# Performance work log

Hardware: AMD Instinct MI355X
Metric: run time of the kernel (lower is better)

Reference implementation:

```python
import jax, jax.numpy as jnp
import numpy as np

SEQ, D, H = 4096, 1024, 16
HD = D // H
SCALE = HD ** -0.5


def setup_inputs() -> dict:
    key = jax.random.key(0)
    ks = jax.random.split(key, 8)
    s = 0.02
    return {
        "hidden_states": jax.random.normal(ks[0], (SEQ, D), dtype=jnp.float32),
        "wq": jax.random.normal(ks[1], (D, D), dtype=jnp.float32) * s,
        "bq": jax.random.normal(ks[2], (D,), dtype=jnp.float32) * s,
        "wk": jax.random.normal(ks[3], (D, D), dtype=jnp.float32) * s,
        "wv": jax.random.normal(ks[4], (D, D), dtype=jnp.float32) * s,
        "bv": jax.random.normal(ks[5], (D,), dtype=jnp.float32) * s,
        "wo": jax.random.normal(ks[6], (D, D), dtype=jnp.float32) * s,
        "bo": jax.random.normal(ks[7], (D,), dtype=jnp.float32) * s,
    }


def reference(hidden_states, wq, bq, wk, wv, bv, wo, bo):
    S = hidden_states.shape[0]
    # torch Linear: y = x @ W^T + b  (k_proj has no bias)
    q = (hidden_states @ wq.T + bq).reshape(S, H, HD).transpose(1, 0, 2)  # [H,S,hd]
    k = (hidden_states @ wk.T).reshape(S, H, HD).transpose(1, 0, 2)       # [H,S,hd]
    v = (hidden_states @ wv.T + bv).reshape(S, H, HD).transpose(1, 0, 2)  # [H,S,hd]
    scores = jnp.einsum('hqd,hkd->hqk', q, k) * SCALE                     # [H,S,S]
    # softmax computed in fp32 then cast back to query dtype
    attn = jax.nn.softmax(scores.astype(jnp.float32), axis=-1).astype(q.dtype)
    out = jnp.einsum('hqk,hkd->hqd', attn, v)                             # [H,S,hd]
    out = out.transpose(1, 0, 2).reshape(S, D)
    return out @ wo.T + bo
```

## Files before the change

### kernel.cpp

```cpp
#include <hip/hip_runtime.h>

#define SEQ 4096
#define DIM 1024
#define NH 16
#define HD 64
#define QKVSTR 3072

typedef __attribute__((ext_vector_type(8))) short bf16x8;
typedef __attribute__((ext_vector_type(4))) float f32x4;
typedef __attribute__((ext_vector_type(16))) float f32x16;
typedef __attribute__((ext_vector_type(4))) unsigned int uint4v;

__device__ __forceinline__ unsigned short f2bf(float f) {
  unsigned int b = __float_as_uint(f);
  b = b + 0x7fffu + ((b >> 16) & 1u);
  return (unsigned short)(b >> 16);
}

__device__ __forceinline__ unsigned int cvt_pk_bf16(float lo, float hi) {
  unsigned int r;
  asm("v_cvt_pk_bf16_f32 %0, %1, %2" : "=v"(r) : "v"(lo), "v"(hi));
  return r;
}

__device__ __forceinline__ float fast_exp2(float x) {
#if __has_builtin(__builtin_amdgcn_exp2f)
  return __builtin_amdgcn_exp2f(x);
#else
  float r; asm("v_exp_f32 %0, %1" : "=v"(r) : "v"(x)); return r;
#endif
}

typedef __attribute__((address_space(3))) unsigned int lds_uint;
typedef __attribute__((address_space(1))) const unsigned int global_uint;

__device__ __forceinline__ void gload_lds16(const void* g, void* l) {
  __builtin_amdgcn_global_load_lds((global_uint*)g, (lds_uint*)l, 16, 0, 0);
}

__global__ __launch_bounds__(256) void cast_all_kernel(
    const float* __restrict__ X, const float* __restrict__ wq, const float* __restrict__ wk,
    const float* __restrict__ wv, const float* __restrict__ wo,
    unsigned short* __restrict__ Xb, unsigned short* __restrict__ Wqkv,
    unsigned short* __restrict__ Wob, float qscale) {
  int i = blockIdx.x * 256 + threadIdx.x;
  const float* src;
  unsigned short* dst;
  float sc = 1.f;
  if (i < 524288) { src = X + (size_t)i * 8; dst = Xb + (size_t)i * 8; }
  else if (i < 655360) { int j = i - 524288; src = wq + (size_t)j * 8; dst = Wqkv + (size_t)j * 8; sc = qscale; }
  else if (i < 786432) { int j = i - 655360; src = wk + (size_t)j * 8; dst = Wqkv + 1048576 + (size_t)j * 8; }
  else if (i < 917504) { int j = i - 786432; src = wv + (size_t)j * 8; dst = Wqkv + 2097152 + (size_t)j * 8; }
  else { int j = i - 917504; src = wo + (size_t)j * 8; dst = Wob + (size_t)j * 8; }
  const float4* p = (const float4*)src;
  float4 x0 = p[0], x1 = p[1];
  union { unsigned short u[8]; uint4v v; } o;
  o.u[0] = f2bf(x0.x * sc); o.u[1] = f2bf(x0.y * sc);
  o.u[2] = f2bf(x0.z * sc); o.u[3] = f2bf(x0.w * sc);
  o.u[4] = f2bf(x1.x * sc); o.u[5] = f2bf(x1.y * sc);
  o.u[6] = f2bf(x1.z * sc); o.u[7] = f2bf(x1.w * sc);
  *(uint4v*)dst = o.v;
}

template<int BIASMODE, int OUT_F32, int BN>
__global__ __launch_bounds__(256) void gemm_bt_kernel(
    const unsigned short* __restrict__ A, const unsigned short* __restrict__ B,
    const float* __restrict__ b0, const float* __restrict__ b1, float qscale,
    void* __restrict__ Cout, unsigned short* __restrict__ Vt, int M, int N, int K) {
  constexpr int NF = BN / 32;
  __shared__ unsigned short As[3][128 * 32];
  __shared__ unsigned short Bs[3][BN * 32];
  int tid = threadIdx.x;
  int wave = tid >> 6, lane = tid & 63;
  int g = lane >> 4, lc = lane & 15;
  int wm = wave >> 1, wn = wave & 1;

  int gx = gridDim.x;
  int wgid = blockIdx.y * gx + blockIdx.x;
  int cpx = (gx * gridDim.y) >> 3;
  int sw = (wgid & 7) * cpx + (wgid >> 3);
  int m0 = (sw / gx) * 128, n0 = (sw % gx) * BN;

  int ch0 = wave * 64 + lane;
  int r0 = ch0 >> 2, cb0 = ch0 & 3;
  int ch1 = 256 + ch0;
  int r1 = ch1 >> 2, cb1 = ch1 & 3;
  const unsigned short* Ar0 = A + (size_t)(m0 + r0) * K + cb0 * 8;
  const unsigned short* Ar1 = A + (size_t)(m0 + r1) * K + cb1 * 8;
  const unsigned short* Br0 = B + (size_t)(n0 + r0) * K + cb0 * 8;
  const unsigned short* Br1 = B + (size_t)(n0 + r1) * K + cb1 * 8;

  unsigned short* sAlo[3] = { &As[0][(wave * 64) * 8], &As[1][(wave * 64) * 8], &As[2][(wave * 64) * 8] };
  unsigned short* sAhi[3] = { &As[0][(256 + wave * 64) * 8], &As[1][(256 + wave * 64) * 8], &As[2][(256 + wave * 64) * 8] };
  unsigned short* sBlo[3] = { &Bs[0][(wave * 64) * 8], &Bs[1][(wave * 64) * 8], &Bs[2][(wave * 64) * 8] };
  unsigned short* sBhi[3] = { &Bs[0][(256 + wave * 64) * 8], &Bs[1][(256 + wave * 64) * 8], &Bs[2][(256 + wave * 64) * 8] };

  f32x4 acc[4][NF] = {};

  auto stage = [&](int kn, int b) {
    gload_lds16(Ar0 + kn, sAlo[b]);
    gload_lds16(Ar1 + kn, sAhi[b]);
    gload_lds16(Br0 + kn, sBlo[b]);
    if (BN == 128) gload_lds16(Br1 + kn, sBhi[b]);
  };

  auto compute = [&](int b) {
    bf16x8 af[4], bfr[NF];
    for (int mf = 0; mf < 4; ++mf)
      af[mf] = *(const bf16x8*)&As[b][(wm * 64 + mf * 16 + lc) * 32 + g * 8];
    for (int nf = 0; nf < NF; ++nf)
      bfr[nf] = *(const bf16x8*)&Bs[b][(wn * (BN / 2) + nf * 16 + lc) * 32 + g * 8];
    for (int mf = 0; mf < 4; ++mf)
      for (int nf = 0; nf < NF; ++nf)
        acc[mf][nf] = __builtin_amdgcn_mfma_f32_16x16x32_bf16(af[mf], bfr[nf], acc[mf][nf], 0, 0, 0);
  };

  const int NT = K / 32;
  auto step = [&](int i, int CUR, int STG) {
    int kn = (i + 2 < NT) ? (i + 2) * 32 : 0;
    stage(kn, STG);
    if (BN == 128) {
      asm volatile("s_waitcnt vmcnt(8)" ::: "memory");
    } else {
      asm volatile("s_waitcnt vmcnt(6)" ::: "memory");
    }
    __builtin_amdgcn_sched_barrier(0);
    __builtin_amdgcn_s_barrier();
    __builtin_amdgcn_sched_barrier(0);
    compute(CUR);
    asm volatile("" ::: "memory");
    __builtin_amdgcn_sched_barrier(0);
    __builtin_amdgcn_s_barrier();
  };

  stage(0, 0);
  stage(32, 1);

  for (int ii = 0; ii < 30; ii += 3) {
    step(ii + 0, 0, 2);
    step(ii + 1, 1, 0);
    step(ii + 2, 2, 1);
  }
  step(30, 0, 2);
  step(31, 1, 0);

  for (int nf = 0; nf < NF; ++nf) {
    int col = n0 + wn * (BN / 2) + nf * 16 + lc;
    float bias = 0.f;
    if (BIASMODE == 1) {
      int sect = col >> 10, cc = col & 1023;
      bias = (sect == 0) ? b0[cc] * qscale : ((sect == 2) ? b1[cc] : 0.f);
    } else if (BIASMODE == 2) {
      bias = b0[col];
    }
    for (int mf = 0; mf < 4; ++mf) {
      int row = m0 + wm * 64 + mf * 16 + g * 4;
      for (int r = 0; r < 4; ++r) {
        float v = acc[mf][nf][r] + bias;
        if (OUT_F32) {
          ((float*)Cout)[(size_t)(row + r) * N + col] = v;
        } else if (BIASMODE == 1 && col >= 2048) {
          Vt[(size_t)(col - 2048) * SEQ + row + r] = f2bf(v);
        } else {
          ((unsigned short*)Cout)[(size_t)(row + r) * N + col] = f2bf(v);
        }
      }
    }
  }
}

__global__ __launch_bounds__(512, 1) void attn_kernel(
    const unsigned short* __restrict__ QKV, const unsigned short* __restrict__ Vt,
    unsigned short* __restrict__ Aout) {
  __shared__ unsigned short Qs[128 * 64];
  __shared__ unsigned short Ks[2][2][64 * 64];
  __shared__ unsigned short Vs[2][2][64 * 64];
  int tid = threadIdx.x;
  int w = tid >> 6, lane = tid & 63;
  int hi = lane >> 5, l31 = lane & 31;
  int qw = w & 3, grp = w >> 2;

  int bid = blockIdx.x;
  int swz = (bid & 7) * 64 + (bid >> 3);
  int h = swz >> 5;
  int q0 = (swz & 31) * 128;

  const unsigned short* Qg = QKV + h * HD;
  const unsigned short* Kg = QKV + DIM + h * HD;
  const unsigned short* Vg = Vt + (size_t)(h * HD) * SEQ;
  int kvbase = grp * (SEQ / 2);

  int ch0 = qw * 64 + lane;
  int r0s = ch0 >> 3, d0s = (ch0 & 7) ^ (r0s & 7);
  int ch1 = 256 + ch0;
  int r1s = ch1 >> 3, d1s = (ch1 & 7) ^ (r1s & 7);
  size_t koff0 = (size_t)r0s * QKVSTR + d0s * 8;
  size_t koff1 = (size_t)r1s * QKVSTR + d1s * 8;
  size_t voff0 = (size_t)r0s * SEQ + d0s * 8;
  size_t voff1 = (size_t)r1s * SEQ + d1s * 8;
  unsigned short* sKlo[2] = { &Ks[grp][0][(qw * 64) * 8],       &Ks[grp][1][(qw * 64) * 8] };
  unsigned short* sKhi[2] = { &Ks[grp][0][(256 + qw * 64) * 8], &Ks[grp][1][(256 + qw * 64) * 8] };
  unsigned short* sVlo[2] = { &Vs[grp][0][(qw * 64) * 8],       &Vs[grp][1][(qw * 64) * 8] };
  unsigned short* sVhi[2] = { &Vs[grp][0][(256 + qw * 64) * 8], &Vs[grp][1][(256 + qw * 64) * 8] };

  for (int c = 0; c < 2; ++c) {
    int chunk = c * 512 + w * 64 + lane;
    int row = chunk >> 3, pos = chunk & 7;
    int db = pos ^ (row & 7);
    gload_lds16(Qg + (size_t)(q0 + row) * QKVSTR + db * 8, Qs + (c * 512 + w * 64) * 8);
  }
  {
    const unsigned short* Kt = Kg + (size_t)kvbase * QKVSTR;
    const unsigned short* Vtt = Vg + kvbase;
    gload_lds16(Kt + koff0, sKlo[0]);
    gload_lds16(Kt + koff1, sKhi[0]);
    gload_lds16(Vtt + voff0, sVlo[0]);
    gload_lds16(Vtt + voff1, sVhi[0]);
  }
  asm volatile("s_waitcnt vmcnt(4)" ::: "memory");
  __builtin_amdgcn_sched_barrier(0);
  __builtin_amdgcn_s_barrier();

  bf16x8 qf[4];
  {
    int qrow = qw * 32 + l31;
    for (int dc = 0; dc < 4; ++dc) {
      int pos = 2 * dc + hi;
      qf[dc] = *(const bf16x8*)&Qs[qrow * 64 + (pos ^ (qrow & 7)) * 8];
    }
  }

  int offb[4];
#pragma unroll
  for (int dc = 0; dc < 4; ++dc)
    offb[dc] = l31 * 128 + (((2 * dc + hi) ^ (l31 & 7)) * 16);
  const char* KbA = (const char*)&Ks[grp][0][0];
  const char* KbB = (const char*)&Ks[grp][1][0];
  const char* VbA = (const char*)&Vs[grp][0][0];
  const char* VbB = (const char*)&Vs[grp][1][0];

  f32x16 o0 = {}, o1 = {};
  float la0 = 0.f, la1 = 0.f, la2 = 0.f, la3 = 0.f;

  auto body = [&](int t, int CUR) {
    int NB = CUR ^ 1;
    int kvn = kvbase + (((t + 1) & 31) << 6);
    const unsigned short* Kt = Kg + (size_t)kvn * QKVSTR;
    const unsigned short* Vtt = Vg + kvn;
    gload_lds16(Kt + koff0, sKlo[NB]);
    gload_lds16(Kt + koff1, sKhi[NB]);
    gload_lds16(Vtt + voff0, sVlo[NB]);
    gload_lds16(Vtt + voff1, sVhi[NB]);
    asm volatile("s_waitcnt vmcnt(4)" ::: "memory");
    __builtin_amdgcn_sched_barrier(0);
    __builtin_amdgcn_s_barrier();
    __builtin_amdgcn_sched_barrier(0);

    const char* Kb = CUR ? KbB : KbA;
    const char* Vb = CUR ? VbB : VbA;
    bf16x8 kf0[4], kf1[4];
#pragma unroll
    for (int dc = 0; dc < 4; ++dc) {
      kf0[dc] = *(const bf16x8*)(Kb + offb[dc]);
      kf1[dc] = *(const bf16x8*)(Kb + offb[dc] + 4096);
    }
    f32x16 st0 = {}, st1 = {};
    __builtin_amdgcn_s_setprio(1);
#pragma unroll
    for (int dc = 0; dc < 4; ++dc) {
      st0 = __builtin_amdgcn_mfma_f32_32x32x16_bf16(kf0[dc], qf[dc], st0, 0, 0, 0);
      st1 = __builtin_amdgcn_mfma_f32_32x32x16_bf16(kf1[dc], qf[dc], st1, 0, 0, 0);
    }
    __builtin_amdgcn_s_setprio(0);

    bf16x8 vf0[4], vf1[4];
#pragma unroll
    for (int c = 0; c < 4; ++c) {
      vf0[c] = *(const bf16x8*)(Vb + offb[c]);
      vf1[c] = *(const bf16x8*)(Vb + offb[c] + 4096);
    }

    float p0[16], p1[16];
#pragma unroll
    for (int r = 0; r < 16; r += 4) {
      p0[r] = fast_exp2(st0[r]); p0[r + 1] = fast_exp2(st0[r + 1]);
      p0[r + 2] = fast_exp2(st0[r + 2]); p0[r + 3] = fast_exp2(st0[r + 3]);
      la0 += p0[r]; la1 += p0[r + 1]; la2 += p0[r + 2]; la3 += p0[r + 3];
    }
#pragma unroll
    for (int r = 0; r < 16; r += 4) {
      p1[r] = fast_exp2(st1[r]); p1[r + 1] = fast_exp2(st1[r + 1]);
      p1[r + 2] = fast_exp2(st1[r + 2]); p1[r + 3] = fast_exp2(st1[r + 3]);
      la0 += p1[r]; la1 += p1[r + 1]; la2 += p1[r + 2]; la3 += p1[r + 3];
    }

    bf16x8 pa[4];
#pragma unroll
    for (int f = 0; f < 2; ++f) {
      const float* pp = f ? p1 : p0;
#pragma unroll
      for (int cc = 0; cc < 2; ++cc) {
        unsigned uLO0 = cvt_pk_bf16(pp[8 * cc + 0], pp[8 * cc + 1]);
        unsigned uLO1 = cvt_pk_bf16(pp[8 * cc + 2], pp[8 * cc + 3]);
        unsigned uHI0 = cvt_pk_bf16(pp[8 * cc + 4], pp[8 * cc + 5]);
        unsigned uHI1 = cvt_pk_bf16(pp[8 * cc + 6], pp[8 * cc + 7]);
        auto s0 = __builtin_amdgcn_permlane32_swap(uLO0, uHI0, false, false);
        auto s1 = __builtin_amdgcn_permlane32_swap(uLO1, uHI1, false, false);
        union { unsigned u[4]; bf16x8 v; } pw;
        pw.u[0] = s0[0]; pw.u[1] = s1[0]; pw.u[2] = s0[1]; pw.u[3] = s1[1];
        pa[f * 2 + cc] = pw.v;
      }
    }

    __builtin_amdgcn_s_setprio(1);
#pragma unroll
    for (int c = 0; c < 4; ++c) {
      o0 = __builtin_amdgcn_mfma_f32_32x32x16_bf16(pa[c], vf0[c], o0, 0, 0, 0);
      o1 = __builtin_amdgcn_mfma_f32_32x32x16_bf16(pa[c], vf1[c], o1, 0, 0, 0);
    }
    __builtin_amdgcn_s_setprio(0);

    asm volatile("" ::: "memory");
    __builtin_amdgcn_sched_barrier(0);
    __builtin_amdgcn_s_barrier();
  };

  for (int tt = 0; tt < 32; tt += 2) {
    body(tt + 0, 0);
    body(tt + 1, 1);
  }

  float lsum = (la0 + la1) + (la2 + la3);
  lsum += __shfl_xor(lsum, 32);

  __syncthreads();
  float* cbO0 = (float*)&Ks[0][0][0];
  float* cbO1 = (float*)&Vs[0][0][0];
  float* cbL  = (float*)&Qs[0];
  int cbase = (qw * 64 + lane) * 32;
  int lx = lane & 31;
  if (grp == 1) {
#pragma unroll
    for (int r = 0; r < 16; ++r) {
      cbO0[cbase + (r ^ lx)] = o0[r];
      cbO1[cbase + (r ^ lx)] = o1[r];
    }
    cbL[qw * 64 + lane] = lsum;
  }
  __syncthreads();
  if (grp == 0) {
#pragma unroll
    for (int r = 0; r < 16; ++r) {
      o0[r] += cbO0[cbase + (r ^ lx)];
      o1[r] += cbO1[cbase + (r ^ lx)];
    }
    lsum += cbL[qw * 64 + lane];
    float inv = 1.f / lsum;
#pragma unroll
    for (int r = 0; r < 16; ++r) {
      int qr = (r & 3) + 8 * (r >> 2) + 4 * hi;
      float ir = __shfl(inv, qr + (lane & 32));
      size_t row = q0 + qw * 32 + qr;
      Aout[row * DIM + h * HD + l31]      = f2bf(o0[r] * ir);
      Aout[row * DIM + h * HD + 32 + l31] = f2bf(o1[r] * ir);
    }
  }
}

extern "C" void kernel_launch(void* const* d_in, const int* in_sizes, int n_in,
                              void* d_out, int out_size, void* d_ws, size_t ws_size,
                              hipStream_t stream) {
  (void)in_sizes; (void)n_in; (void)out_size; (void)ws_size;
  const float* X  = (const float*)d_in[0];
  const float* wq = (const float*)d_in[1];
  const float* bq = (const float*)d_in[2];
  const float* wk = (const float*)d_in[3];
  const float* wv = (const float*)d_in[4];
  const float* bv = (const float*)d_in[5];
  const float* wo = (const float*)d_in[6];
  const float* bo = (const float*)d_in[7];

  char* ws = (char*)d_ws;
  const size_t SZ_XD  = (size_t)SEQ * DIM * 2;
  const size_t SZ_W   = (size_t)DIM * DIM * 2;
  const size_t SZ_QKV = (size_t)SEQ * QKVSTR * 2;
  unsigned short* Xb   = (unsigned short*)(ws);
  unsigned short* Wqkv = (unsigned short*)(ws + SZ_XD);
  unsigned short* Wob  = (unsigned short*)(ws + SZ_XD + 3 * SZ_W);
  unsigned short* QKVb = (unsigned short*)(ws + SZ_XD + 4 * SZ_W);
  unsigned short* Vtb  = (unsigned short*)(ws + SZ_XD + 4 * SZ_W + SZ_QKV);
  unsigned short* Ab   = Xb;

  const float QSCALE = 0.125f * 1.44269504088896f;

  cast_all_kernel<<<4096, 256, 0, stream>>>(X, wq, wk, wv, wo, Xb, Wqkv, Wob, QSCALE);

  gemm_bt_kernel<1, 0, 128><<<dim3(QKVSTR / 128, SEQ / 128), 256, 0, stream>>>(
      Xb, Wqkv, bq, bv, QSCALE, QKVb, Vtb, SEQ, QKVSTR, DIM);

  attn_kernel<<<SEQ / 128 * NH, 512, 0, stream>>>(QKVb, Vtb, Ab);

  gemm_bt_kernel<2, 1, 64><<<dim3(DIM / 64, SEQ / 128), 256, 0, stream>>>(
      Ab, Wob, bo, nullptr, 1.f, d_out, nullptr, SEQ, DIM, DIM);
}
```

Measured before the change: 159.7 us.

## Halve attention KV tile to 32 keys and shrink shared memory footprint

The attention kernel now streams 32-key K/V tiles instead of 64-key tiles, doubling the loop trip count. Per iteration it issues one QK MFMA chain and two PV MFMA pairs. K and V go into a single flat 48 KB shared buffer, with V using a 4-way XOR swizzle. The cross-group output reduction is split into two passes that reuse the same scratch region. This cuts LDS use and register pressure, but doubles the number of barriers and loop iterations and gives less MFMA work between syncs.

```diff
diff --git a/kernel.cpp b/kernel.cpp
--- a/kernel.cpp
+++ b/kernel.cpp
@@ -172,9 +172,8 @@
 __global__ __launch_bounds__(512, 1) void attn_kernel(
     const unsigned short* __restrict__ QKV, const unsigned short* __restrict__ Vt,
     unsigned short* __restrict__ Aout) {
-  __shared__ unsigned short Qs[128 * 64];
-  __shared__ unsigned short Ks[2][2][64 * 64];
-  __shared__ unsigned short Vs[2][2][64 * 64];
+  __shared__ unsigned short SMEM[24576];
+  unsigned short* Qs = SMEM;
   int tid = threadIdx.x;
   int w = tid >> 6, lane = tid & 63;
   int hi = lane >> 5, l31 = lane & 31;
@@ -190,18 +189,19 @@
   const unsigned short* Vg = Vt + (size_t)(h * HD) * SEQ;
   int kvbase = grp * (SEQ / 2);
 
-  int ch0 = qw * 64 + lane;
-  int r0s = ch0 >> 3, d0s = (ch0 & 7) ^ (r0s & 7);
-  int ch1 = 256 + ch0;
-  int r1s = ch1 >> 3, d1s = (ch1 & 7) ^ (r1s & 7);
-  size_t koff0 = (size_t)r0s * QKVSTR + d0s * 8;
-  size_t koff1 = (size_t)r1s * QKVSTR + d1s * 8;
-  size_t voff0 = (size_t)r0s * SEQ + d0s * 8;
-  size_t voff1 = (size_t)r1s * SEQ + d1s * 8;
-  unsigned short* sKlo[2] = { &Ks[grp][0][(qw * 64) * 8],       &Ks[grp][1][(qw * 64) * 8] };
-  unsigned short* sKhi[2] = { &Ks[grp][0][(256 + qw * 64) * 8], &Ks[grp][1][(256 + qw * 64) * 8] };
-  unsigned short* sVlo[2] = { &Vs[grp][0][(qw * 64) * 8],       &Vs[grp][1][(qw * 64) * 8] };
-  unsigned short* sVhi[2] = { &Vs[grp][0][(256 + qw * 64) * 8], &Vs[grp][1][(256 + qw * 64) * 8] };
+  unsigned short* Kt0 = SMEM + 8192 + (grp * 2 + 0) * 2048;
+  unsigned short* Kt1 = SMEM + 8192 + (grp * 2 + 1) * 2048;
+  unsigned short* Vt0 = SMEM + 16384 + (grp * 2 + 0) * 2048;
+  unsigned short* Vt1 = SMEM + 16384 + (grp * 2 + 1) * 2048;
+
+  int ch = qw * 64 + lane;
+  int krow = ch >> 3, kpos = (ch & 7) ^ (krow & 7);
+  int vrow = ch >> 2, vpos = (ch & 3) ^ (vrow & 3);
+  size_t koff = (size_t)krow * QKVSTR + kpos * 8;
+  size_t voff = (size_t)vrow * SEQ + vpos * 8;
+  unsigned short* sK[2] = { Kt0 + ch * 8 - lane * 8 + lane * 8, Kt1 + ch * 8 - lane * 8 + lane * 8 };
+  unsigned short* sKb[2] = { Kt0 + (qw * 64) * 8, Kt1 + (qw * 64) * 8 };
+  unsigned short* sVb[2] = { Vt0 + (qw * 64) * 8, Vt1 + (qw * 64) * 8 };
 
   for (int c = 0; c < 2; ++c) {
     int chunk = c * 512 + w * 64 + lane;
@@ -209,15 +209,9 @@
     int db = pos ^ (row & 7);
     gload_lds16(Qg + (size_t)(q0 + row) * QKVSTR + db * 8, Qs + (c * 512 + w * 64) * 8);
   }
-  {
-    const unsigned short* Kt = Kg + (size_t)kvbase * QKVSTR;
-    const unsigned short* Vtt = Vg + kvbase;
-    gload_lds16(Kt + koff0, sKlo[0]);
-    gload_lds16(Kt + koff1, sKhi[0]);
-    gload_lds16(Vtt + voff0, sVlo[0]);
-    gload_lds16(Vtt + voff1, sVhi[0]);
-  }
-  asm volatile("s_waitcnt vmcnt(4)" ::: "memory");
+  gload_lds16(Kg + (size_t)kvbase * QKVSTR + koff, sKb[0]);
+  gload_lds16(Vg + kvbase + voff, sVb[0]);
+  asm volatile("s_waitcnt vmcnt(2)" ::: "memory");
   __builtin_amdgcn_sched_barrier(0);
   __builtin_amdgcn_s_barrier();
 
@@ -230,91 +224,76 @@
     }
   }
 
-  int offb[4];
+  int kOffb[4], vOffb[2];
 #pragma unroll
   for (int dc = 0; dc < 4; ++dc)
-    offb[dc] = l31 * 128 + (((2 * dc + hi) ^ (l31 & 7)) * 16);
-  const char* KbA = (const char*)&Ks[grp][0][0];
-  const char* KbB = (const char*)&Ks[grp][1][0];
-  const char* VbA = (const char*)&Vs[grp][0][0];
-  const char* VbB = (const char*)&Vs[grp][1][0];
+    kOffb[dc] = l31 * 128 + (((2 * dc + hi) ^ (l31 & 7)) * 16);
+#pragma unroll
+  for (int c = 0; c < 2; ++c)
+    vOffb[c] = l31 * 64 + (((2 * c + hi) ^ (l31 & 3)) * 16);
+  const char* KbA = (const char*)Kt0;
+  const char* KbB = (const char*)Kt1;
+  const char* VbA = (const char*)Vt0;
+  const char* VbB = (const char*)Vt1;
 
   f32x16 o0 = {}, o1 = {};
   float la0 = 0.f, la1 = 0.f, la2 = 0.f, la3 = 0.f;
 
   auto body = [&](int t, int CUR) {
     int NB = CUR ^ 1;
-    int kvn = kvbase + (((t + 1) & 31) << 6);
-    const unsigned short* Kt = Kg + (size_t)kvn * QKVSTR;
-    const unsigned short* Vtt = Vg + kvn;
-    gload_lds16(Kt + koff0, sKlo[NB]);
-    gload_lds16(Kt + koff1, sKhi[NB]);
-    gload_lds16(Vtt + voff0, sVlo[NB]);
-    gload_lds16(Vtt + voff1, sVhi[NB]);
-    asm volatile("s_waitcnt vmcnt(4)" ::: "memory");
+    int kvn = kvbase + (((t + 1) & 63) << 5);
+    gload_lds16(Kg + (size_t)kvn * QKVSTR + koff, sKb[NB]);
+    gload_lds16(Vg + kvn + voff, sVb[NB]);
+    asm volatile("s_waitcnt vmcnt(2)" ::: "memory");
     __builtin_amdgcn_sched_barrier(0);
     __builtin_amdgcn_s_barrier();
     __builtin_amdgcn_sched_barrier(0);
 
     const char* Kb = CUR ? KbB : KbA;
     const char* Vb = CUR ? VbB : VbA;
-    bf16x8 kf0[4], kf1[4];
-#pragma unroll
-    for (int dc = 0; dc < 4; ++dc) {
-      kf0[dc] = *(const bf16x8*)(Kb + offb[dc]);
-      kf1[dc] = *(const bf16x8*)(Kb + offb[dc] + 4096);
-    }
-    f32x16 st0 = {}, st1 = {};
+    bf16x8 kf[4];
+#pragma unroll
+    for (int dc = 0; dc < 4; ++dc)
+      kf[dc] = *(const bf16x8*)(Kb + kOffb[dc]);
+    f32x16 st0 = {};
     __builtin_amdgcn_s_setprio(1);
 #pragma unroll
-    for (int dc = 0; dc < 4; ++dc) {
-      st0 = __builtin_amdgcn_mfma_f32_32x32x16_bf16(kf0[dc], qf[dc], st0, 0, 0, 0);
-      st1 = __builtin_amdgcn_mfma_f32_32x32x16_bf16(kf1[dc], qf[dc], st1, 0, 0, 0);
-    }
+    for (int dc = 0; dc < 4; ++dc)
+      st0 = __builtin_amdgcn_mfma_f32_32x32x16_bf16(kf[dc], qf[dc], st0, 0, 0, 0);
     __builtin_amdgcn_s_setprio(0);
 
-    bf16x8 vf0[4], vf1[4];
-#pragma unroll
-    for (int c = 0; c < 4; ++c) {
-      vf0[c] = *(const bf16x8*)(Vb + offb[c]);
-      vf1[c] = *(const bf16x8*)(Vb + offb[c] + 4096);
-    }
-
-    float p0[16], p1[16];
+    bf16x8 vf0[2], vf1[2];
+#pragma unroll
+    for (int c = 0; c < 2; ++c) {
+      vf0[c] = *(const bf16x8*)(Vb + vOffb[c]);
+      vf1[c] = *(const bf16x8*)(Vb + vOffb[c] + 2048);
+    }
+
+    float p0[16];
 #pragma unroll
     for (int r = 0; r < 16; r += 4) {
       p0[r] = fast_exp2(st0[r]); p0[r + 1] = fast_exp2(st0[r + 1]);
       p0[r + 2] = fast_exp2(st0[r + 2]); p0[r + 3] = fast_exp2(st0[r + 3]);
       la0 += p0[r]; la1 += p0[r + 1]; la2 += p0[r + 2]; la3 += p0[r + 3];
     }
-#pragma unroll
-    for (int r = 0; r < 16; r += 4) {
-      p1[r] = fast_exp2(st1[r]); p1[r + 1] = fast_exp2(st1[r + 1]);
-      p1[r + 2] = fast_exp2(st1[r + 2]); p1[r + 3] = fast_exp2(st1[r + 3]);
-      la0 += p1[r]; la1 += p1[r + 1]; la2 += p1[r + 2]; la3 += p1[r + 3];
-    }
-
-    bf16x8 pa[4];
-#pragma unroll
-    for (int f = 0; f < 2; ++f) {
-      const float* pp = f ? p1 : p0;
-#pragma unroll
-      for (int cc = 0; cc < 2; ++cc) {
-        unsigned uLO0 = cvt_pk_bf16(pp[8 * cc + 0], pp[8 * cc + 1]);
-        unsigned uLO1 = cvt_pk_bf16(pp[8 * cc + 2], pp[8 * cc + 3]);
-        unsigned uHI0 = cvt_pk_bf16(pp[8 * cc + 4], pp[8 * cc + 5]);
-        unsigned uHI1 = cvt_pk_bf16(pp[8 * cc + 6], pp[8 * cc + 7]);
-        auto s0 = __builtin_amdgcn_permlane32_swap(uLO0, uHI0, false, false);
-        auto s1 = __builtin_amdgcn_permlane32_swap(uLO1, uHI1, false, false);
-        union { unsigned u[4]; bf16x8 v; } pw;
-        pw.u[0] = s0[0]; pw.u[1] = s1[0]; pw.u[2] = s0[1]; pw.u[3] = s1[1];
-        pa[f * 2 + cc] = pw.v;
-      }
+
+    bf16x8 pa[2];
+#pragma unroll
+    for (int cc = 0; cc < 2; ++cc) {
+      unsigned uLO0 = cvt_pk_bf16(p0[8 * cc + 0], p0[8 * cc + 1]);
+      unsigned uLO1 = cvt_pk_bf16(p0[8 * cc + 2], p0[8 * cc + 3]);
+      unsigned uHI0 = cvt_pk_bf16(p0[8 * cc + 4], p0[8 * cc + 5]);
+      unsigned uHI1 = cvt_pk_bf16(p0[8 * cc + 6], p0[8 * cc + 7]);
+      auto s0 = __builtin_amdgcn_permlane32_swap(uLO0, uHI0, false, false);
+      auto s1 = __builtin_amdgcn_permlane32_swap(uLO1, uHI1, false, false);
+      union { unsigned u[4]; bf16x8 v; } pw;
+      pw.u[0] = s0[0]; pw.u[1] = s1[0]; pw.u[2] = s0[1]; pw.u[3] = s1[1];
+      pa[cc] = pw.v;
     }
 
     __builtin_amdgcn_s_setprio(1);
 #pragma unroll
-    for (int c = 0; c < 4; ++c) {
+    for (int c = 0; c < 2; ++c) {
       o0 = __builtin_amdgcn_mfma_f32_32x32x16_bf16(pa[c], vf0[c], o0, 0, 0, 0);
       o1 = __builtin_amdgcn_mfma_f32_32x32x16_bf16(pa[c], vf1[c], o1, 0, 0, 0);
     }
@@ -325,7 +304,7 @@
     __builtin_amdgcn_s_barrier();
   };
 
-  for (int tt = 0; tt < 32; tt += 2) {
+  for (int tt = 0; tt < 64; tt += 2) {
     body(tt + 0, 0);
     body(tt + 1, 1);
   }
@@ -333,28 +312,31 @@
   float lsum = (la0 + la1) + (la2 + la3);
   lsum += __shfl_xor(lsum, 32);
 
-  __syncthreads();
-  float* cbO0 = (float*)&Ks[0][0][0];
-  float* cbO1 = (float*)&Vs[0][0][0];
-  float* cbL  = (float*)&Qs[0];
+  float* cb = (float*)SMEM;
+  float* cbL = (float*)(SMEM + 16384);
   int cbase = (qw * 64 + lane) * 32;
   int lx = lane & 31;
+  __syncthreads();
   if (grp == 1) {
 #pragma unroll
-    for (int r = 0; r < 16; ++r) {
-      cbO0[cbase + (r ^ lx)] = o0[r];
-      cbO1[cbase + (r ^ lx)] = o1[r];
-    }
+    for (int r = 0; r < 16; ++r) cb[cbase + (r ^ lx)] = o0[r];
     cbL[qw * 64 + lane] = lsum;
   }
   __syncthreads();
   if (grp == 0) {
 #pragma unroll
-    for (int r = 0; r < 16; ++r) {
-      o0[r] += cbO0[cbase + (r ^ lx)];
-      o1[r] += cbO1[cbase + (r ^ lx)];
-    }
+    for (int r = 0; r < 16; ++r) o0[r] += cb[cbase + (r ^ lx)];
     lsum += cbL[qw * 64 + lane];
+  }
+  __syncthreads();
+  if (grp == 1) {
+#pragma unroll
+    for (int r = 0; r < 16; ++r) cb[cbase + (r ^ lx)] = o1[r];
+  }
+  __syncthreads();
+  if (grp == 0) {
+#pragma unroll
+    for (int r = 0; r < 16; ++r) o1[r] += cb[cbase + (r ^ lx)];
     float inv = 1.f / lsum;
 #pragma unroll
     for (int r = 0; r < 16; ++r) {
```

Measured after the change: 152.6 us. 4.5% less time.
